# Optimization experiments

Measured on AMD Instinct MI355X. Metric: run time of the kernel, lower is better.

## Reference

```python
import jax, jax.numpy as jnp
import numpy as np


def setup_inputs() -> dict:
    key = jax.random.key(0)
    ks = jax.random.split(key, 5)
    B, D, L, NH = 2, 1024, 2048, 8
    H = D // NH  # number of SSM heads / filter channels
    return {
        "v": jax.random.normal(ks[0], (B, D, L), jnp.float32),
        "k": jax.random.normal(ks[1], (H, L), jnp.float32) * 0.1,
        "bias": jax.random.normal(ks[2], (D,), jnp.float32),
        "x1": jax.random.normal(ks[3], (B, D, L), jnp.float32),
        "x2": jax.random.normal(ks[4], (B, D, L), jnp.float32),
        "num_heads": NH,
    }


def reference(v, k, bias, x1, x2, num_heads):
    # Multi-head Hyena FFT long conv with fused gating (safari fftconv_h3 semantics):
    #   kv[b,h,d1,d2,l] = v[b,h,d1,l] * x2[b,h,d2,l]
    #   y = causal_fftconv(kv, k[h]) + bias[h,d1] * kv
    #   out[b,h,d2,l] = sum_d1 y[b,h,d1,d2,l] * x1[b,h,d1,l]
    B, D, L = v.shape
    H = D // num_heads
    fft_size = 2 * L  # zero-pad to 2L for linear (causal) convolution
    vr = v.reshape(B, H, num_heads, L)
    x1r = x1.reshape(B, H, num_heads, L)
    x2r = x2.reshape(B, H, num_heads, L)
    kv = vr[:, :, :, None, :] * x2r[:, :, None, :, :]  # (B, H, d1, d2, L)
    k_f = jnp.fft.rfft(k.astype(jnp.float32), n=fft_size)  # (H, fft_size//2+1)
    y = jnp.fft.irfft(
        jnp.fft.rfft(kv, n=fft_size) * k_f[None, :, None, None, :], n=fft_size
    )[..., :L]  # (B, H, d1, d2, L)
    skip = bias.astype(jnp.float32).reshape(H, num_heads)[None, :, :, None, None]
    y = y + kv * skip
    out = jnp.einsum("bhijl,bhil->bhjl", y, x1r)  # contract d1 with q-gate
    return out.reshape(B, D, L)
```

## Files before the change

### kernel.cpp

```cpp
#include <hip/hip_runtime.h>
#include <stdint.h>


typedef __attribute__((ext_vector_type(8))) short bf16x8;
typedef __attribute__((ext_vector_type(4))) float f32x4;
typedef __attribute__((ext_vector_type(2))) float f32x2;

#define NHd  8
#define SC   128
#define GW   256

static __device__ __forceinline__ uint32_t pkbf(float a, float b) {
    const uint32_t ua = __float_as_uint(a) + 0x8000u;
    const uint32_t ub = __float_as_uint(b) + 0x8000u;
    return __builtin_amdgcn_perm(ub, ua, 0x07060302u);
}

static __device__ __forceinline__ uint32_t pktr(f32x2 p) {
    union { f32x2 f; uint32_t u[2]; } c; c.f = p;
    return __builtin_amdgcn_perm(c.u[1], c.u[0], 0x07060302u);
}

static __device__ __forceinline__ uint32_t gmul2(f32x2 s, f32x2 g) {
    return pktr(s * g);
}

union U8 { uint32_t u[4]; bf16x8 v; uint4 q; };

__global__ __launch_bounds__(256, 5) void hyena_mfma10_kernel(
    const float* __restrict__ v, const float* __restrict__ kf,
    const float* __restrict__ bias, const float* __restrict__ x1,
    const float* __restrict__ x2, float* __restrict__ out,
    int B, int H, int L)
{
    __shared__ __align__(16) float  ks[2048];
    __shared__ __align__(16) float4 gwin[GW];
    __shared__ __align__(16) ushort vT[2][SC][NHd];
    __shared__ __align__(16) ushort x2T[2][NHd][136];
    __shared__ float sbuf[2][128];

    const int tid  = threadIdx.x;
    const int h    = blockIdx.x;
    const int l0b  = ((int)gridDim.y - 1 - (int)blockIdx.y) * 128;
    const int nk   = l0b + 128;

    const int lane = tid & 63, wv = tid >> 6;
    const int lq   = lane & 15, quad = lane >> 4;
    const int wb   = wv & 1;
    const int wseg = wv >> 1;
    const int wl0  = l0b + wseg * 64;
    const int baseb = (wb * H + h) * NHd * L;

    for (int i = tid; i < nk; i += 256) ks[i] = kf[h * L + i];

    bf16x8 xf[4] = {};
    if (quad == 0) {
#pragma unroll
        for (int j = 0; j < 4; ++j) {
            float a0[NHd];
#pragma unroll
            for (int d1 = 0; d1 < NHd; ++d1)
                a0[d1] = x1[baseb + d1 * L + wl0 + 16 * j + lq];
            U8 u0;
#pragma unroll
            for (int t = 0; t < 4; ++t) u0.u[t] = pkbf(a0[2 * t], a0[2 * t + 1]);
            xf[j] = u0.v;
        }
    }

    {
        const int bb = tid >> 7, l = tid & 127;
        const int bs = (bb * H + h) * NHd * L;
        float s = 0.f;
#pragma unroll
        for (int d1 = 0; d1 < NHd; ++d1)
            s += bias[h * NHd + d1] * x1[bs + d1 * L + l0b + l]
                                    * v [bs + d1 * L + l0b + l];
        sbuf[bb][l] = s;
    }

    f32x4 acc[4];
#pragma unroll
    for (int j = 0; j < 4; ++j) acc[j] = (f32x4){0.f, 0.f, 0.f, 0.f};

    const int wlmax = wl0 + 63;
    const int ebase = 127 + wseg * 64 + lq - 4 * quad;

    bool gfirst = true;
    float4 g0, g1, g2, g3, g4;

    for (int s0 = 0; s0 < nk; s0 += SC) {
        __syncthreads();
        {
            const int bb = tid >> 7, row = tid & 127;
            const int bs = (bb * H + h) * NHd * L;
            const float* vp = v + bs + s0 + row;
            float f[NHd];
#pragma unroll
            for (int d1 = 0; d1 < NHd; ++d1) f[d1] = vp[d1 * L];
            *(uint4*)&vT[bb][row][0] = make_uint4(
                pkbf(f[0], f[1]), pkbf(f[2], f[3]),
                pkbf(f[4], f[5]), pkbf(f[6], f[7]));

            const int d2 = row >> 4, ms = (row & 15) * 8;
            const int G = ms & ~31;
            const int o = ms & 31;
            const int pa = ((o >> 2) & 3) * 8 + (o >> 4) * 4;
            const float* xp = x2 + bs + d2 * L + s0 + ms;
            const float4 q0 = *(const float4*)xp;
            const float4 q1 = *(const float4*)(xp + 4);
            *(uint2*)&x2T[bb][d2][G + pa] =
                make_uint2(pkbf(q0.x, q0.y), pkbf(q0.z, q0.w));
            *(uint2*)&x2T[bb][d2][G + pa + 8] =
                make_uint2(pkbf(q1.x, q1.y), pkbf(q1.z, q1.w));
        }
        if (tid < GW - 1) {
            const int i = l0b - s0 - 127 + tid;
            float4 w = {0.f, 0.f, 0.f, 0.f};
            if (i >= 3) {
                w.x = ks[i]; w.y = ks[i - 1]; w.z = ks[i - 2]; w.w = ks[i - 3];
            } else if (i >= 0) {
                w.x = ks[i];
                if (i >= 1) w.y = ks[i - 1];
                if (i >= 2) w.z = ks[i - 2];
            }
            gwin[tid] = w;
        }
        __syncthreads();

        const int cmax = min(SC, wlmax - s0 + 1);
        for (int c = 0; c < cmax; c += 32) {
            const int e = ebase - c;

            bf16x8 av0 = {}, av1 = {};
            if (quad == 0) {
                av0 = *(const bf16x8*)&vT[wb][c + lq][0];
                av1 = *(const bf16x8*)&vT[wb][c + 16 + lq][0];
            }
            if (gfirst) {
                g4 = *(const float4*)&gwin[e + 48];
                g3 = *(const float4*)&gwin[e + 32];
                g2 = *(const float4*)&gwin[e + 16];
                gfirst = false;
            } else { g4 = g2; g3 = g1; g2 = g0; }
            g1 = *(const float4*)&gwin[e];
            g0 = *(const float4*)&gwin[e - 16];
            const bf16x8 ax = *(const bf16x8*)&x2T[wb][lq & 7][c + 8 * quad];

            const f32x4 Z = {0.f, 0.f, 0.f, 0.f};
            {
                const f32x4 Sa0 = __builtin_amdgcn_mfma_f32_16x16x32_bf16(av0, xf[0], Z, 0, 0, 0);
                const f32x4 Sa1 = __builtin_amdgcn_mfma_f32_16x16x32_bf16(av1, xf[0], Z, 0, 0, 0);
                const f32x4 Sb0 = __builtin_amdgcn_mfma_f32_16x16x32_bf16(av0, xf[1], Z, 0, 0, 0);
                const f32x4 Sb1 = __builtin_amdgcn_mfma_f32_16x16x32_bf16(av1, xf[1], Z, 0, 0, 0);
                U8 p;
                p.u[0] = gmul2((f32x2){Sa0[0], Sa0[1]}, (f32x2){g1.x, g1.y});
                p.u[1] = gmul2((f32x2){Sa0[2], Sa0[3]}, (f32x2){g1.z, g1.w});
                p.u[2] = gmul2((f32x2){Sa1[0], Sa1[1]}, (f32x2){g0.x, g0.y});
                p.u[3] = gmul2((f32x2){Sa1[2], Sa1[3]}, (f32x2){g0.z, g0.w});
                acc[0] = __builtin_amdgcn_mfma_f32_16x16x32_bf16(ax, p.v, acc[0], 0, 0, 0);
                p.u[0] = gmul2((f32x2){Sb0[0], Sb0[1]}, (f32x2){g2.x, g2.y});
                p.u[1] = gmul2((f32x2){Sb0[2], Sb0[3]}, (f32x2){g2.z, g2.w});
                p.u[2] = gmul2((f32x2){Sb1[0], Sb1[1]}, (f32x2){g1.x, g1.y});
                p.u[3] = gmul2((f32x2){Sb1[2], Sb1[3]}, (f32x2){g1.z, g1.w});
                acc[1] = __builtin_amdgcn_mfma_f32_16x16x32_bf16(ax, p.v, acc[1], 0, 0, 0);
            }
            {
                const f32x4 Sc0 = __builtin_amdgcn_mfma_f32_16x16x32_bf16(av0, xf[2], Z, 0, 0, 0);
                const f32x4 Sc1 = __builtin_amdgcn_mfma_f32_16x16x32_bf16(av1, xf[2], Z, 0, 0, 0);
                const f32x4 Sd0 = __builtin_amdgcn_mfma_f32_16x16x32_bf16(av0, xf[3], Z, 0, 0, 0);
                const f32x4 Sd1 = __builtin_amdgcn_mfma_f32_16x16x32_bf16(av1, xf[3], Z, 0, 0, 0);
                U8 p;
                p.u[0] = gmul2((f32x2){Sc0[0], Sc0[1]}, (f32x2){g3.x, g3.y});
                p.u[1] = gmul2((f32x2){Sc0[2], Sc0[3]}, (f32x2){g3.z, g3.w});
                p.u[2] = gmul2((f32x2){Sc1[0], Sc1[1]}, (f32x2){g2.x, g2.y});
                p.u[3] = gmul2((f32x2){Sc1[2], Sc1[3]}, (f32x2){g2.z, g2.w});
                acc[2] = __builtin_amdgcn_mfma_f32_16x16x32_bf16(ax, p.v, acc[2], 0, 0, 0);
                p.u[0] = gmul2((f32x2){Sd0[0], Sd0[1]}, (f32x2){g4.x, g4.y});
                p.u[1] = gmul2((f32x2){Sd0[2], Sd0[3]}, (f32x2){g4.z, g4.w});
                p.u[2] = gmul2((f32x2){Sd1[0], Sd1[1]}, (f32x2){g3.x, g3.y});
                p.u[3] = gmul2((f32x2){Sd1[2], Sd1[3]}, (f32x2){g3.z, g3.w});
                acc[3] = __builtin_amdgcn_mfma_f32_16x16x32_bf16(ax, p.v, acc[3], 0, 0, 0);
            }
        }
    }

    if (quad < 2) {
#pragma unroll
        for (int j = 0; j < 4; ++j) {
            const int lA  = wl0 + 16 * j + lq;
            const float sb = sbuf[wb][wseg * 64 + 16 * j + lq];
#pragma unroll
            for (int r = 0; r < 4; ++r) {
                const int ro = baseb + (4 * quad + r) * L + lA;
                out[ro] = acc[j][r] + x2[ro] * sb;
            }
        }
    }
}

extern "C" void kernel_launch(void* const* d_in, const int* in_sizes, int n_in,
                              void* d_out, int out_size, void* d_ws, size_t ws_size,
                              hipStream_t stream) {
    const float* v    = (const float*)d_in[0];
    const float* k    = (const float*)d_in[1];
    const float* bias = (const float*)d_in[2];
    const float* x1   = (const float*)d_in[3];
    const float* x2   = (const float*)d_in[4];
    float* out = (float*)d_out;

    const int D = in_sizes[2];
    const int H = D / NHd;
    const int L = in_sizes[1] / H;
    const int B = in_sizes[0] / (D * L);

    dim3 grid(H, L / 128);
    hyena_mfma10_kernel<<<grid, 256, 0, stream>>>(v, k, bias, x1, x2, out, B, H, L);
}
```

Before: 151.1 us.

## Prefetch next stage into registers and drop the shared filter copy

Global loads of v, x2 and the filter taps for the next chunk are issued into registers before the compute loop of the current chunk, so their latency overlaps with the MFMA work. The 8 KB shared ks buffer is removed and the filter window is read straight from global memory. This frees LDS, and the occupancy hint is raised from 5 to 6 blocks per SM. The custom waitcnt/barrier pairs only wait on LDS, which relies on the compiler to insert vmcnt waits before the prefetched registers are used. Register pressure rises.

Result: slower. 296.4 us (+96.2%).

```diff
diff --git a/kernel.cpp b/kernel.cpp
--- a/kernel.cpp
+++ b/kernel.cpp
@@ -27,13 +27,12 @@
 
 union U8 { uint32_t u[4]; bf16x8 v; uint4 q; };
 
-__global__ __launch_bounds__(256, 5) void hyena_mfma10_kernel(
+__global__ __launch_bounds__(256, 6) void hyena_mfma11_kernel(
     const float* __restrict__ v, const float* __restrict__ kf,
     const float* __restrict__ bias, const float* __restrict__ x1,
     const float* __restrict__ x2, float* __restrict__ out,
     int B, int H, int L)
 {
-    __shared__ __align__(16) float  ks[2048];
     __shared__ __align__(16) float4 gwin[GW];
     __shared__ __align__(16) ushort vT[2][SC][NHd];
     __shared__ __align__(16) ushort x2T[2][NHd][136];
@@ -51,7 +50,41 @@
     const int wl0  = l0b + wseg * 64;
     const int baseb = (wb * H + h) * NHd * L;
 
-    for (int i = tid; i < nk; i += 256) ks[i] = kf[h * L + i];
+    const int sb_b   = tid >> 7, sb_row = tid & 127;
+    const int sb_bs  = (sb_b * H + h) * NHd * L;
+    const float* vp0 = v + sb_bs + sb_row;
+    const int sb_d2  = sb_row >> 4, sb_ms = (sb_row & 15) * 8;
+    const int sb_G   = sb_ms & ~31;
+    const int sb_o   = sb_ms & 31;
+    const int sb_pa  = ((sb_o >> 2) & 3) * 8 + (sb_o >> 4) * 4;
+    const float* xp0 = x2 + sb_bs + sb_d2 * L + sb_ms;
+    const float* kp  = kf + h * L;
+    const int gi0    = l0b - 127 + tid;
+
+    float  fv0, fv1, fv2, fv3, fv4, fv5, fv6, fv7;
+    float4 q0, q1;
+    float  kg0 = 0.f, kg1 = 0.f, kg2 = 0.f, kg3 = 0.f;
+
+    auto issue_stage = [&](int s0) {
+        const float* vp = vp0 + s0;
+        fv0 = vp[0 * L]; fv1 = vp[1 * L]; fv2 = vp[2 * L]; fv3 = vp[3 * L];
+        fv4 = vp[4 * L]; fv5 = vp[5 * L]; fv6 = vp[6 * L]; fv7 = vp[7 * L];
+        q0 = *(const float4*)(xp0 + s0);
+        q1 = *(const float4*)(xp0 + s0 + 4);
+        if (tid < GW - 1) {
+            const int i = gi0 - s0;
+            if (i >= 3) {
+                kg0 = kp[i]; kg1 = kp[i - 1]; kg2 = kp[i - 2]; kg3 = kp[i - 3];
+            } else {
+                kg0 = kg1 = kg2 = kg3 = 0.f;
+                if (i >= 0) kg0 = kp[i];
+                if (i >= 1) kg1 = kp[i - 1];
+                if (i >= 2) kg2 = kp[i - 2];
+            }
+        }
+    };
+
+    issue_stage(0);
 
     bf16x8 xf[4] = {};
     if (quad == 0) {
@@ -90,43 +123,22 @@
     float4 g0, g1, g2, g3, g4;
 
     for (int s0 = 0; s0 < nk; s0 += SC) {
-        __syncthreads();
-        {
-            const int bb = tid >> 7, row = tid & 127;
-            const int bs = (bb * H + h) * NHd * L;
-            const float* vp = v + bs + s0 + row;
-            float f[NHd];
-#pragma unroll
-            for (int d1 = 0; d1 < NHd; ++d1) f[d1] = vp[d1 * L];
-            *(uint4*)&vT[bb][row][0] = make_uint4(
-                pkbf(f[0], f[1]), pkbf(f[2], f[3]),
-                pkbf(f[4], f[5]), pkbf(f[6], f[7]));
-
-            const int d2 = row >> 4, ms = (row & 15) * 8;
-            const int G = ms & ~31;
-            const int o = ms & 31;
-            const int pa = ((o >> 2) & 3) * 8 + (o >> 4) * 4;
-            const float* xp = x2 + bs + d2 * L + s0 + ms;
-            const float4 q0 = *(const float4*)xp;
-            const float4 q1 = *(const float4*)(xp + 4);
-            *(uint2*)&x2T[bb][d2][G + pa] =
-                make_uint2(pkbf(q0.x, q0.y), pkbf(q0.z, q0.w));
-            *(uint2*)&x2T[bb][d2][G + pa + 8] =
-                make_uint2(pkbf(q1.x, q1.y), pkbf(q1.z, q1.w));
-        }
-        if (tid < GW - 1) {
-            const int i = l0b - s0 - 127 + tid;
-            float4 w = {0.f, 0.f, 0.f, 0.f};
-            if (i >= 3) {
-                w.x = ks[i]; w.y = ks[i - 1]; w.z = ks[i - 2]; w.w = ks[i - 3];
-            } else if (i >= 0) {
-                w.x = ks[i];
-                if (i >= 1) w.y = ks[i - 1];
-                if (i >= 2) w.z = ks[i - 2];
-            }
-            gwin[tid] = w;
-        }
-        __syncthreads();
+        asm volatile("s_waitcnt lgkmcnt(0)" ::: "memory");
+        __builtin_amdgcn_s_barrier();
+
+        *(uint4*)&vT[sb_b][sb_row][0] = make_uint4(
+            pkbf(fv0, fv1), pkbf(fv2, fv3), pkbf(fv4, fv5), pkbf(fv6, fv7));
+        *(uint2*)&x2T[sb_b][sb_d2][sb_G + sb_pa] =
+            make_uint2(pkbf(q0.x, q0.y), pkbf(q0.z, q0.w));
+        *(uint2*)&x2T[sb_b][sb_d2][sb_G + sb_pa + 8] =
+            make_uint2(pkbf(q1.x, q1.y), pkbf(q1.z, q1.w));
+        if (tid < GW - 1)
+            gwin[tid] = make_float4(kg0, kg1, kg2, kg3);
+
+        if (s0 + SC < nk) issue_stage(s0 + SC);
+
+        asm volatile("s_waitcnt lgkmcnt(0)" ::: "memory");
+        __builtin_amdgcn_s_barrier();
 
         const int cmax = min(SC, wlmax - s0 + 1);
         for (int c = 0; c < cmax; c += 32) {
@@ -215,5 +227,5 @@
     const int B = in_sizes[0] / (D * L);
 
     dim3 grid(H, L / 128);
-    hyena_mfma10_kernel<<<grid, 256, 0, stream>>>(v, k, bias, x1, x2, out, B, H, L);
-}
+    hyena_mfma11_kernel<<<grid, 256, 0, stream>>>(v, k, bias, x1, x2, out, B, H, L);
+}
```
